# Performance work log

Hardware: AMD Instinct MI355X
Metric: run time of the kernel (lower is better)

Reference implementation:

```python
import jax, jax.numpy as jnp
import numpy as np

B, S, D, F, E, K = 4, 2048, 768, 3072, 8, 2
LB_W, Z_W = 0.01, 0.001


def setup_inputs() -> dict:
    key = jax.random.key(0)
    ks = jax.random.split(key, 6)
    x = jax.random.normal(ks[0], (B, S, D), dtype=jnp.float32)
    Wr = jax.random.truncated_normal(ks[1], -2.0, 2.0, (D, E), dtype=jnp.float32) * 0.02
    W1 = jax.random.normal(ks[2], (E, D, F), dtype=jnp.float32) * (1.0 / np.sqrt(D))
    b1 = jnp.zeros((E, F), dtype=jnp.float32)
    W2 = jax.random.normal(ks[3], (E, F, D), dtype=jnp.float32) * (1.0 / np.sqrt(F))
    b2 = jnp.zeros((E, D), dtype=jnp.float32)
    return {"x": x, "Wr": Wr, "W1": W1, "b1": b1, "W2": W2, "b2": b2}


def reference(x, Wr, W1, b1, W2, b2):
    # Router
    router_logits = jnp.einsum('bsd,de->bse', x, Wr)            # [B,S,E]
    router_probs = jax.nn.softmax(router_logits, axis=-1)
    top_k_probs, top_k_idx = jax.lax.top_k(router_probs, K)     # [B,S,K]
    top_k_probs = top_k_probs / (jnp.sum(top_k_probs, axis=-1, keepdims=True) + 1e-8)

    # Auxiliary losses
    expert_usage = jnp.mean(router_probs, axis=(0, 1))          # [E]
    mean_usage = jnp.mean(expert_usage)
    var_usage = jnp.mean(jnp.square(expert_usage - mean_usage))
    lb_loss = var_usage / (mean_usage * mean_usage + 1e-8) * jnp.float32(E)
    z_loss = jnp.mean(jnp.square(jax.nn.logsumexp(router_logits, axis=-1)))

    # Combine weights per expert: sum over top-k slots assigned to expert e
    one_hot = jax.nn.one_hot(top_k_idx, E, dtype=x.dtype)       # [B,S,K,E]
    combine = jnp.sum(one_hot * top_k_probs[..., None], axis=2) # [B,S,E]

    # Expert FFNs (loop over fixed small E, vectorized over tokens)
    output = jnp.zeros_like(x)
    for e in range(E):
        h = jax.nn.gelu(jnp.einsum('bsd,df->bsf', x, W1[e]) + b1[e], approximate=False)
        y = jnp.einsum('bsf,fd->bsd', h, W2[e]) + b2[e]
        output = output + y * combine[..., e:e + 1]

    aux = {"load_balancing_loss": lb_loss * LB_W, "router_z_loss": z_loss * Z_W}
    return output, aux["load_balancing_loss"], aux["router_z_loss"]
```

## Files before the change

### kernel.cpp

```cpp
#include <hip/hip_runtime.h>
#include <cstdint>
#include <cstddef>

#define B_ 4
#define S_ 2048
#define D_ 768
#define F_ 3072
#define E_ 8
#define NTOK (B_*S_)
#define NASSIGN (NTOK*2)
#define RBLK 256
#define FBLK 32
#define MAXTILE 136

typedef unsigned short u16;
typedef __attribute__((ext_vector_type(8))) __bf16 bf16x8;
typedef __attribute__((ext_vector_type(4))) float f32x4;

__device__ __forceinline__ u16 f2bf(float f) {
    unsigned int u = __builtin_bit_cast(unsigned int, f);
    u += 0x7fffu + ((u >> 16) & 1u);
    return (u16)(u >> 16);
}

__device__ __forceinline__ void async16(const void* g, void* l) {
    __builtin_amdgcn_global_load_lds(
        (const __attribute__((address_space(1))) unsigned int*)g,
        (__attribute__((address_space(3))) unsigned int*)l, 16, 0, 0);
}

__device__ __forceinline__ float gelu_f(float v) {
    float z = v * 0.70710678f;
    float a = fabsf(z);
    float t = __builtin_amdgcn_rcpf(1.0f + 0.3275911f * a);
    float poly = t * (0.254829592f + t * (-0.284496736f + t * (1.421413741f +
                 t * (-1.453152027f + t * 1.061405429f))));
    float e = __expf(-z * z);
    float erf_z = copysignf(1.0f - poly * e, z);
    return 0.5f * v * (1.0f + erf_z);
}

__global__ void k_cvt_x(const float* __restrict__ x, u16* __restrict__ xb) {
    int id = blockIdx.x * 256 + threadIdx.x;
    float4 v = ((const float4*)x)[id];
    ushort4 o;
    o.x = f2bf(v.x); o.y = f2bf(v.y); o.z = f2bf(v.z); o.w = f2bf(v.w);
    ((ushort4*)xb)[id] = o;
}

__global__ __launch_bounds__(256) void k_tcvt(const float* __restrict__ in, u16* __restrict__ out, int R, int C) {
    __shared__ u16 t[64][72];
    int e = blockIdx.z;
    int c0 = blockIdx.x * 64, r0 = blockIdx.y * 64;
    int tid = threadIdx.x;
    int sx = tid & 15;
    int sy = tid >> 4;
    const float* ip = in + (size_t)e * R * C + (size_t)(r0 + sy * 4) * C + c0 + sx * 4;
    float4 v0 = *(const float4*)(ip);
    float4 v1 = *(const float4*)(ip + C);
    float4 v2 = *(const float4*)(ip + 2 * (size_t)C);
    float4 v3 = *(const float4*)(ip + 3 * (size_t)C);
    ushort4 o;
    o.x = f2bf(v0.x); o.y = f2bf(v1.x); o.z = f2bf(v2.x); o.w = f2bf(v3.x);
    *(ushort4*)&t[sx * 4 + 0][sy * 4] = o;
    o.x = f2bf(v0.y); o.y = f2bf(v1.y); o.z = f2bf(v2.y); o.w = f2bf(v3.y);
    *(ushort4*)&t[sx * 4 + 1][sy * 4] = o;
    o.x = f2bf(v0.z); o.y = f2bf(v1.z); o.z = f2bf(v2.z); o.w = f2bf(v3.z);
    *(ushort4*)&t[sx * 4 + 2][sy * 4] = o;
    o.x = f2bf(v0.w); o.y = f2bf(v1.w); o.z = f2bf(v2.w); o.w = f2bf(v3.w);
    *(ushort4*)&t[sx * 4 + 3][sy * 4] = o;
    __syncthreads();
    int od = tid & 7;
    int oc = tid >> 3;
    u16* obase = out + (size_t)e * C * R;
    #pragma unroll
    for (int p = 0; p < 2; p++) {
        int c = oc + p * 32;
        *(uint4*)(obase + (size_t)(c0 + c) * R + r0 + od * 8) = *(const uint4*)&t[c][od * 8];
    }
}

__global__ __launch_bounds__(256) void k_router(
    const float* __restrict__ x, const float* __restrict__ Wr,
    float* __restrict__ usage_part, float* __restrict__ z_part,
    int* __restrict__ hist_part,
    int* __restrict__ tk_idx, float* __restrict__ tk_w)
{
    __shared__ float wrt[E_ * D_];
    __shared__ float s_usage[E_];
    __shared__ float s_z;
    __shared__ int   s_hist[E_];
    int tid = threadIdx.x;
    for (int i = tid; i < E_ * D_; i += 256) {
        int d = i >> 3, e = i & 7;
        wrt[e * D_ + d] = Wr[i];
    }
    if (tid < E_) { s_usage[tid] = 0.f; s_hist[tid] = 0; }
    if (tid == 0) s_z = 0.f;
    __syncthreads();

    int w = tid >> 6, lane = tid & 63;
    float u_acc[E_];
    #pragma unroll
    for (int e = 0; e < E_; e++) u_acc[e] = 0.f;
    float z_acc = 0.f;

    for (int it = 0; it < 8; it++) {
        int tok = blockIdx.x * 32 + it * 4 + w;
        float acc[E_];
        #pragma unroll
        for (int e = 0; e < E_; e++) acc[e] = 0.f;
        const float* xr = x + (size_t)tok * D_;
        for (int d = lane; d < D_; d += 64) {
            float xv = xr[d];
            #pragma unroll
            for (int e = 0; e < E_; e++) acc[e] += xv * wrt[e * D_ + d];
        }
        #pragma unroll
        for (int off = 32; off > 0; off >>= 1) {
            #pragma unroll
            for (int e = 0; e < E_; e++) acc[e] += __shfl_down(acc[e], off);
        }
        if (lane == 0) {
            float m = acc[0];
            #pragma unroll
            for (int e = 1; e < E_; e++) m = fmaxf(m, acc[e]);
            float p[E_], s = 0.f;
            #pragma unroll
            for (int e = 0; e < E_; e++) { p[e] = expf(acc[e] - m); s += p[e]; }
            float inv = 1.f / s;
            #pragma unroll
            for (int e = 0; e < E_; e++) { p[e] *= inv; u_acc[e] += p[e]; }
            float lse = m + logf(s);
            z_acc += lse * lse;
            int i1 = 0;
            for (int e = 1; e < E_; e++) if (p[e] > p[i1]) i1 = e;
            int i2 = -1;
            for (int e = 0; e < E_; e++) {
                if (e == i1) continue;
                if (i2 < 0 || p[e] > p[i2]) i2 = e;
            }
            float denom = p[i1] + p[i2] + 1e-8f;
            tk_idx[tok * 2 + 0] = i1; tk_idx[tok * 2 + 1] = i2;
            tk_w[tok * 2 + 0] = p[i1] / denom;
            tk_w[tok * 2 + 1] = p[i2] / denom;
            atomicAdd(&s_hist[i1], 1); atomicAdd(&s_hist[i2], 1);
        }
    }
    if (lane == 0) {
        #pragma unroll
        for (int e = 0; e < E_; e++) atomicAdd(&s_usage[e], u_acc[e]);
        atomicAdd(&s_z, z_acc);
    }
    __syncthreads();
    if (tid < E_) {
        usage_part[blockIdx.x * E_ + tid] = s_usage[tid];
        hist_part[blockIdx.x * E_ + tid]  = s_hist[tid];
    }
    if (tid == 0) z_part[blockIdx.x] = s_z;
}

__global__ __launch_bounds__(256) void k_finalize(
    const float* __restrict__ usage_part, const float* __restrict__ z_part,
    const int* __restrict__ hist_part,
    int* __restrict__ counts, int* __restrict__ offsets,
    int* __restrict__ cursors,
    int* __restrict__ tile_list,
    float* __restrict__ out_scalars)
{
    __shared__ float s_u[E_];
    __shared__ float s_z;
    __shared__ int   s_h[E_];
    int tid = threadIdx.x;
    if (tid < E_) { s_u[tid] = 0.f; s_h[tid] = 0; cursors[tid] = 0; }
    if (tid == 0) s_z = 0.f;
    __syncthreads();

    float u[E_]; int h[E_];
    #pragma unroll
    for (int e = 0; e < E_; e++) { u[e] = usage_part[tid * E_ + e]; h[e] = hist_part[tid * E_ + e]; }
    float z = z_part[tid];
    #pragma unroll
    for (int off = 32; off > 0; off >>= 1) {
        #pragma unroll
        for (int e = 0; e < E_; e++) {
            u[e] += __shfl_down(u[e], off);
            h[e] += __shfl_down(h[e], off);
        }
        z += __shfl_down(z, off);
    }
    if ((tid & 63) == 0) {
        #pragma unroll
        for (int e = 0; e < E_; e++) { atomicAdd(&s_u[e], u[e]); atomicAdd(&s_h[e], h[e]); }
        atomicAdd(&s_z, z);
    }
    __syncthreads();
    if (tid == 0) {
        int o = 0, nt = 0;
        for (int e = 0; e < E_; e++) {
            int c = s_h[e];
            counts[e] = c; offsets[e] = o; o += c;
            for (int m0 = 0; m0 < c; m0 += 128) tile_list[1 + nt++] = (m0 << 8) | e;
        }
        tile_list[0] = nt;
        float uu[E_], mean = 0.f;
        for (int e = 0; e < E_; e++) { uu[e] = s_u[e] / (float)NTOK; mean += uu[e]; }
        mean /= (float)E_;
        float var = 0.f;
        for (int e = 0; e < E_; e++) { float d = uu[e] - mean; var += d * d; }
        var /= (float)E_;
        out_scalars[0] = var / (mean * mean + 1e-8f) * (float)E_ * 0.01f;
        out_scalars[1] = (s_z / (float)NTOK) * 0.001f;
    }
}

__global__ __launch_bounds__(256) void k_fill(
    const int* __restrict__ tk_idx, const float* __restrict__ tk_w,
    const int* __restrict__ offsets, int* __restrict__ cursors,
    int* __restrict__ assign_token, float* __restrict__ assign_weight)
{
    __shared__ int l_cnt[E_];
    __shared__ int l_base[E_];
    int tid = threadIdx.x;
    if (tid < E_) l_cnt[tid] = 0;
    __syncthreads();
    int t = blockIdx.x * 256 + tid;
    int e0 = tk_idx[t * 2 + 0], e1 = tk_idx[t * 2 + 1];
    int r0 = atomicAdd(&l_cnt[e0], 1);
    int r1 = atomicAdd(&l_cnt[e1], 1);
    __syncthreads();
    if (tid < E_) l_base[tid] = atomicAdd(&cursors[tid], l_cnt[tid]);
    __syncthreads();
    int row0 = offsets[e0] + l_base[e0] + r0;
    int row1 = offsets[e1] + l_base[e1] + r1;
    assign_token[row0] = t; assign_weight[row0] = tk_w[t * 2 + 0];
    assign_token[row1] = t; assign_weight[row1] = tk_w[t * 2 + 1];
}

__global__ __launch_bounds__(256) void k_gemm1(
    const u16* __restrict__ xb, const u16* __restrict__ w1t,
    const float* __restrict__ b1,
    const int* __restrict__ counts, const int* __restrict__ offsets,
    const int* __restrict__ tile_list,
    const int* __restrict__ assign_token, u16* __restrict__ h)
{
    int bid = blockIdx.x;
    int xcd = bid & 7;
    int j = bid >> 3;
    int nx = j / 17;
    int mt = xcd * 17 + (j % 17);
    int nt = tile_list[0];
    if (mt >= nt) return;
    int packed = tile_list[1 + mt];
    int e = packed & 0xff;
    int m0 = packed >> 8;
    int cnt = counts[e];
    int off = offsets[e];
    int n0 = nx * 128;

    __shared__ __align__(16) u16 SM[16384];
    char* smb = (char*)SM;

    int tid = threadIdx.x;
    int w = tid >> 6, lane = tid & 63;
    int rA = lane >> 2;
    int colk = ((lane & 3) ^ (rA & 3)) * 8;
    int r0 = (w * 2 + 0) * 16 + rA;
    int r1 = (w * 2 + 1) * 16 + rA;

    int c0b = __builtin_amdgcn_readfirstlane((w * 2 + 0) * 1024);
    int c1b = __builtin_amdgcn_readfirstlane((w * 2 + 1) * 1024);

    int g0 = m0 + r0; if (g0 > cnt - 1) g0 = cnt - 1;
    int g1 = m0 + r1; if (g1 > cnt - 1) g1 = cnt - 1;
    const u16* agp0 = xb + (size_t)assign_token[off + g0] * D_ + colk;
    const u16* agp1 = xb + (size_t)assign_token[off + g1] * D_ + colk;
    const u16* bgp0 = w1t + ((size_t)e * F_ + n0 + r0) * D_ + colk;
    const u16* bgp1 = w1t + ((size_t)e * F_ + n0 + r1) * D_ + colk;

    f32x4 acc[4][4];
    #pragma unroll
    for (int i = 0; i < 4; i++)
        #pragma unroll
        for (int j2 = 0; j2 < 4; j2++) acc[i][j2] = (f32x4){0.f, 0.f, 0.f, 0.f};

    int wm = (w >> 1) * 64, wn = (w & 1) * 64;
    int fm = lane & 15;
    int slot = ((lane >> 4) ^ (fm & 3)) * 8;

    #define STAGE1(buf, kk) do { \
        async16(agp0 + (kk), smb + (buf) * 8192 + c0b); \
        async16(agp1 + (kk), smb + (buf) * 8192 + c1b); \
        async16(bgp0 + (kk), smb + 16384 + (buf) * 8192 + c0b); \
        async16(bgp1 + (kk), smb + 16384 + (buf) * 8192 + c1b); \
    } while (0)
    #define COMPUTE1(buf) do { \
        const u16* Ab = SM + (buf) * 4096; \
        const u16* Bb = SM + 8192 + (buf) * 4096; \
        bf16x8 af[4], bfr[4]; \
        _Pragma("unroll") \
        for (int i = 0; i < 4; i++) af[i] = *(const bf16x8*)&Ab[(wm + i * 16 + fm) * 32 + slot]; \
        _Pragma("unroll") \
        for (int j2 = 0; j2 < 4; j2++) bfr[j2] = *(const bf16x8*)&Bb[(wn + j2 * 16 + fm) * 32 + slot]; \
        _Pragma("unroll") \
        for (int i = 0; i < 4; i++) \
            _Pragma("unroll") \
            for (int j2 = 0; j2 < 4; j2++) \
                acc[i][j2] = __builtin_amdgcn_mfma_f32_16x16x32_bf16(af[i], bfr[j2], acc[i][j2], 0, 0, 0); \
    } while (0)

    STAGE1(0, 0);
    __syncthreads();
    for (int kk = 0; kk < D_; kk += 64) {
        STAGE1(1, kk + 32);
        COMPUTE1(0);
        __syncthreads();
        if (kk + 64 < D_) STAGE1(0, kk + 64);
        COMPUTE1(1);
        __syncthreads();
    }
    #undef STAGE1
    #undef COMPUTE1

    int rbase = (lane >> 4) * 4;
    u16* tb = SM + w * 4096;
    float biasv[4];
    #pragma unroll
    for (int j2 = 0; j2 < 4; j2++) biasv[j2] = b1[e * F_ + n0 + wn + j2 * 16 + fm];
    #pragma unroll
    for (int i = 0; i < 4; i++)
        #pragma unroll
        for (int j2 = 0; j2 < 4; j2++)
            #pragma unroll
            for (int r = 0; r < 4; r++) {
                int m_l = i * 16 + rbase + r;
                int f_l = j2 * 16 + fm;
                u16 q = f2bf(gelu_f(acc[i][j2][r] + biasv[j2]));
                tb[m_l * 64 + ((((f_l >> 3) ^ (m_l & 7)) << 3) | (f_l & 7))] = q;
            }
    __syncthreads();
    #pragma unroll
    for (int s = 0; s < 8; s++) {
        int m_l = s * 8 + (lane >> 3);
        int c = lane & 7;
        uint4 vv = *(const uint4*)&tb[m_l * 64 + ((c ^ (m_l & 7)) << 3)];
        int m = m0 + wm + m_l;
        if (m < cnt)
            *(uint4*)&h[(size_t)(off + m) * F_ + n0 + wn + c * 8] = vv;
    }
}

__global__ __launch_bounds__(256) void k_gemm2(
    const u16* __restrict__ h, const u16* __restrict__ w2t,
    const float* __restrict__ b2,
    const int* __restrict__ counts, const int* __restrict__ offsets,
    const int* __restrict__ tile_list,
    const int* __restrict__ assign_token, const float* __restrict__ assign_weight,
    float* __restrict__ out)
{
    int bid = blockIdx.x;
    int xcd = bid & 7;
    int j = bid >> 3;
    int nx = j % 6;
    int mt = xcd * 17 + (j / 6);
    int nt = tile_list[0];
    if (mt >= nt) return;
    int packed = tile_list[1 + mt];
    int e = packed & 0xff;
    int m0 = packed >> 8;
    int cnt = counts[e];
    int off = offsets[e];
    int n0 = nx * 128;

    __shared__ __align__(16) u16 SM[16384];
    char* smb = (char*)SM;

    int tid = threadIdx.x;
    int w = tid >> 6, lane = tid & 63;
    int rA = lane >> 2;
    int colk = ((lane & 3) ^ (rA & 3)) * 8;
    int r0 = (w * 2 + 0) * 16 + rA;
    int r1 = (w * 2 + 1) * 16 + rA;

    int c0b = __builtin_amdgcn_readfirstlane((w * 2 + 0) * 1024);
    int c1b = __builtin_amdgcn_readfirstlane((w * 2 + 1) * 1024);

    const u16* agp0 = h + (size_t)(off + m0 + r0) * F_ + colk;
    const u16* agp1 = h + (size_t)(off + m0 + r1) * F_ + colk;
    const u16* bgp0 = w2t + ((size_t)e * D_ + n0 + r0) * F_ + colk;
    const u16* bgp1 = w2t + ((size_t)e * D_ + n0 + r1) * F_ + colk;

    f32x4 acc[4][4];
    #pragma unroll
    for (int i = 0; i < 4; i++)
        #pragma unroll
        for (int j2 = 0; j2 < 4; j2++) acc[i][j2] = (f32x4){0.f, 0.f, 0.f, 0.f};

    int wm = (w >> 1) * 64, wn = (w & 1) * 64;
    int fm = lane & 15;
    int slot = ((lane >> 4) ^ (fm & 3)) * 8;

    #define STAGE2(buf, kk) do { \
        async16(agp0 + (kk), smb + (buf) * 8192 + c0b); \
        async16(agp1 + (kk), smb + (buf) * 8192 + c1b); \
        async16(bgp0 + (kk), smb + 16384 + (buf) * 8192 + c0b); \
        async16(bgp1 + (kk), smb + 16384 + (buf) * 8192 + c1b); \
    } while (0)
    #define COMPUTE2(buf) do { \
        const u16* Ab = SM + (buf) * 4096; \
        const u16* Bb = SM + 8192 + (buf) * 4096; \
        bf16x8 af[4], bfr[4]; \
        _Pragma("unroll") \
        for (int i = 0; i < 4; i++) af[i] = *(const bf16x8*)&Ab[(wm + i * 16 + fm) * 32 + slot]; \
        _Pragma("unroll") \
        for (int j2 = 0; j2 < 4; j2++) bfr[j2] = *(const bf16x8*)&Bb[(wn + j2 * 16 + fm) * 32 + slot]; \
        _Pragma("unroll") \
        for (int i = 0; i < 4; i++) \
            _Pragma("unroll") \
            for (int j2 = 0; j2 < 4; j2++) \
                acc[i][j2] = __builtin_amdgcn_mfma_f32_16x16x32_bf16(af[i], bfr[j2], acc[i][j2], 0, 0, 0); \
    } while (0)

    STAGE2(0, 0);
    __syncthreads();
    for (int kk = 0; kk < F_; kk += 64) {
        STAGE2(1, kk + 32);
        COMPUTE2(0);
        __syncthreads();
        if (kk + 64 < F_) STAGE2(0, kk + 64);
        COMPUTE2(1);
        __syncthreads();
    }
    #undef STAGE2
    #undef COMPUTE2

    int rbase = (lane >> 4) * 4;
    float biasv[4];
    #pragma unroll
    for (int j2 = 0; j2 < 4; j2++) biasv[j2] = b2[e * D_ + n0 + wn + j2 * 16 + fm];
    #pragma unroll
    for (int i = 0; i < 4; i++)
        #pragma unroll
        for (int r = 0; r < 4; r++) {
            int m = m0 + wm + i * 16 + rbase + r;
            if (m < cnt) {
                int t = assign_token[off + m];
                float wg = assign_weight[off + m];
                float* orow = out + (size_t)t * D_ + n0 + wn + fm;
                #pragma unroll
                for (int j2 = 0; j2 < 4; j2++)
                    unsafeAtomicAdd(orow + j2 * 16, (acc[i][j2][r] + biasv[j2]) * wg);
            }
        }
}

extern "C" void kernel_launch(void* const* d_in, const int* in_sizes, int n_in,
                              void* d_out, int out_size, void* d_ws, size_t ws_size,
                              hipStream_t stream)
{
    const float* x  = (const float*)d_in[0];
    const float* Wr = (const float*)d_in[1];
    const float* W1 = (const float*)d_in[2];
    const float* b1 = (const float*)d_in[3];
    const float* W2 = (const float*)d_in[4];
    const float* b2 = (const float*)d_in[5];
    float* out = (float*)d_out;

    char* base = (char*)d_ws;
    size_t o = 0;
    auto alloc = [&](size_t bytes) {
        char* r = base + o;
        o += (bytes + 255) & ~(size_t)255;
        return r;
    };
    int*   counts        = (int*)  alloc(E_ * 4);
    int*   cursors       = (int*)  alloc(E_ * 4);
    int*   offsets       = (int*)  alloc(E_ * 4);
    int*   tile_list     = (int*)  alloc(256 * 4);
    float* usage_part    = (float*)alloc((size_t)RBLK * E_ * 4);
    float* z_part        = (float*)alloc((size_t)RBLK * 4);
    int*   hist_part     = (int*)  alloc((size_t)RBLK * E_ * 4);
    int*   tk_idx        = (int*)  alloc((size_t)NTOK * 2 * 4);
    float* tk_w          = (float*)alloc((size_t)NTOK * 2 * 4);
    int*   assign_token  = (int*)  alloc((size_t)NASSIGN * 4);
    float* assign_weight = (float*)alloc((size_t)NASSIGN * 4);
    u16*   xb            = (u16*)  alloc((size_t)NTOK * D_ * 2);
    u16*   w1t           = (u16*)  alloc((size_t)E_ * F_ * D_ * 2);
    u16*   w2t           = (u16*)  alloc((size_t)E_ * D_ * F_ * 2);
    u16*   hbuf          = (u16*)  alloc((size_t)(NASSIGN + 128) * F_ * 2);

    hipMemsetAsync(d_out, 0, (size_t)out_size * 4, stream);
    k_cvt_x<<<dim3(NTOK * D_ / 1024), dim3(256), 0, stream>>>(x, xb);
    k_tcvt<<<dim3(F_ / 64, D_ / 64, E_), dim3(256), 0, stream>>>(W1, w1t, D_, F_);
    k_tcvt<<<dim3(D_ / 64, F_ / 64, E_), dim3(256), 0, stream>>>(W2, w2t, F_, D_);
    k_router<<<dim3(RBLK), dim3(256), 0, stream>>>(x, Wr, usage_part, z_part, hist_part, tk_idx, tk_w);
    k_finalize<<<dim3(1), dim3(256), 0, stream>>>(usage_part, z_part, hist_part, counts, offsets,
                                                  cursors, tile_list, out + (size_t)NTOK * D_);
    k_fill<<<dim3(FBLK), dim3(256), 0, stream>>>(tk_idx, tk_w, offsets, cursors, assign_token, assign_weight);
    k_gemm1<<<dim3(8 * 17 * (F_ / 128)), dim3(256), 0, stream>>>(xb, w1t, b1, counts, offsets, tile_list,
                                                                 assign_token, hbuf);
    k_gemm2<<<dim3(8 * 17 * (D_ / 128)), dim3(256), 0, stream>>>(hbuf, w2t, b2, counts, offsets, tile_list,
                                                                 assign_token, assign_weight, out);
}
```

Baseline: 604.0 us.

## Split-K the second expert GEMM and balance M-tiles evenly across XCDs

The second expert GEMM now splits the F reduction into two halves, doubling the grid. Each half atomically adds its partial result into the output, and only the first half adds the bias. Both GEMMs also spread the variable number of M-tiles evenly over the 8 XCDs instead of packing 17 per XCD, so fewer blocks return early and XCD load is more even. The cost is twice the atomic adds into the output and more blocks each doing shorter K loops.

```diff
diff --git a/kernel.cpp b/kernel.cpp
--- a/kernel.cpp
+++ b/kernel.cpp
@@ -38,6 +38,13 @@
     float e = __expf(-z * z);
     float erf_z = copysignf(1.0f - poly * e, z);
     return 0.5f * v * (1.0f + erf_z);
+}
+
+__device__ __forceinline__ int xcd_tile(int xcd, int mloc, int nt, int* ok) {
+    int q = nt >> 3, r = nt & 7;
+    int cntx = q + (xcd < r ? 1 : 0);
+    *ok = (mloc < cntx);
+    return xcd * q + (xcd < r ? xcd : r) + mloc;
 }
 
 __global__ void k_cvt_x(const float* __restrict__ x, u16* __restrict__ xb) {
@@ -248,9 +255,11 @@
     int xcd = bid & 7;
     int j = bid >> 3;
     int nx = j / 17;
-    int mt = xcd * 17 + (j % 17);
+    int mloc = j % 17;
     int nt = tile_list[0];
-    if (mt >= nt) return;
+    int ok;
+    int mt = xcd_tile(xcd, mloc, nt, &ok);
+    if (!ok) return;
     int packed = tile_list[1 + mt];
     int e = packed & 0xff;
     int m0 = packed >> 8;
@@ -361,16 +370,22 @@
     int bid = blockIdx.x;
     int xcd = bid & 7;
     int j = bid >> 3;
-    int nx = j % 6;
-    int mt = xcd * 17 + (j / 6);
+    int mloc = j / 12;
+    int rem = j % 12;
+    int nx = rem % 6;
+    int kh = rem / 6;
     int nt = tile_list[0];
-    if (mt >= nt) return;
+    int ok;
+    int mt = xcd_tile(xcd, mloc, nt, &ok);
+    if (!ok) return;
     int packed = tile_list[1 + mt];
     int e = packed & 0xff;
     int m0 = packed >> 8;
     int cnt = counts[e];
     int off = offsets[e];
     int n0 = nx * 128;
+    int kbase = kh * (F_ / 2);
+    int kend = kbase + F_ / 2;
 
     __shared__ __align__(16) u16 SM[16384];
     char* smb = (char*)SM;
@@ -421,13 +436,13 @@
                 acc[i][j2] = __builtin_amdgcn_mfma_f32_16x16x32_bf16(af[i], bfr[j2], acc[i][j2], 0, 0, 0); \
     } while (0)
 
-    STAGE2(0, 0);
-    __syncthreads();
-    for (int kk = 0; kk < F_; kk += 64) {
+    STAGE2(0, kbase);
+    __syncthreads();
+    for (int kk = kbase; kk < kend; kk += 64) {
         STAGE2(1, kk + 32);
         COMPUTE2(0);
         __syncthreads();
-        if (kk + 64 < F_) STAGE2(0, kk + 64);
+        if (kk + 64 < kend) STAGE2(0, kk + 64);
         COMPUTE2(1);
         __syncthreads();
     }
@@ -437,7 +452,8 @@
     int rbase = (lane >> 4) * 4;
     float biasv[4];
     #pragma unroll
-    for (int j2 = 0; j2 < 4; j2++) biasv[j2] = b2[e * D_ + n0 + wn + j2 * 16 + fm];
+    for (int j2 = 0; j2 < 4; j2++)
+        biasv[j2] = (kh == 0) ? b2[e * D_ + n0 + wn + j2 * 16 + fm] : 0.f;
     #pragma unroll
     for (int i = 0; i < 4; i++)
         #pragma unroll
@@ -499,6 +515,6 @@
     k_fill<<<dim3(FBLK), dim3(256), 0, stream>>>(tk_idx, tk_w, offsets, cursors, assign_token, assign_weight);
     k_gemm1<<<dim3(8 * 17 * (F_ / 128)), dim3(256), 0, stream>>>(xb, w1t, b1, counts, offsets, tile_list,
                                                                  assign_token, hbuf);
-    k_gemm2<<<dim3(8 * 17 * (D_ / 128)), dim3(256), 0, stream>>>(hbuf, w2t, b2, counts, offsets, tile_list,
-                                                                 assign_token, assign_weight, out);
-}
+    k_gemm2<<<dim3(8 * 17 * (D_ / 128) * 2), dim3(256), 0, stream>>>(hbuf, w2t, b2, counts, offsets, tile_list,
+                                                                     assign_token, assign_weight, out);
+}
```

After: 616.7 us. +2.1%, slower.
